# Optimization experiments

Hardware: AMD Instinct MI355X
Metric: run time of the kernel (lower is better)

Reference implementation:

```python
import jax, jax.numpy as jnp
import numpy as np

ANCHORS = np.array([[10,13],[16,30],[33,23],[30,61],[62,45],[59,119],[116,90],[156,198],[373,326]], dtype=np.float32)
MASKS = [[0,1,2],[3,4,5],[6,7,8]]
H = W = 608
NC = 80
B = 8
GRIDS = [76, 38, 19]
POS_PER_SCALE = 40


def setup_inputs() -> dict:
    key = jax.random.key(0)
    ks = jax.random.split(key, 3)
    rng = np.random.default_rng(0)
    inp = {}
    truths = []
    for i, g in enumerate(GRIDS):
        inp[f"y_out{i}"] = jax.random.normal(ks[i], (B, g, g, 3 * (5 + NC)), dtype=jnp.float32)
        t = rng.random((B, g, g, 3, 5 + NC)).astype(np.float32)
        t[..., 4] = 0.0  # objectness flag: mostly background
        flat = rng.choice(B * g * g * 3, size=POS_PER_SCALE, replace=False)
        bi, yi, xi, ai = np.unravel_index(flat, (B, g, g, 3))
        t[bi, yi, xi, ai, 4] = 1.0
        truths.append(t)
        inp[f"y_truth{i}"] = jnp.asarray(t)
    # same math as the torch code: concat over scales of truth boxes where obj==1
    gtb = np.concatenate([t[t[..., 4] == 1][:, :4] for t in truths], axis=0)
    inp["gtboxes"] = jnp.asarray(gtb)  # (120, 4)
    return inp


def _process(y, mask_idx):
    # decode raw net output -> (b, gy, gx, 3, 5+NC) normalized boxes + sigmoided obj/cls
    b, gy, gx, _ = y.shape
    out = y.reshape(b, gy, gx, 3, 5 + NC)
    a = jnp.asarray(ANCHORS[MASKS[mask_idx]])  # (3, 2)
    xx = jnp.arange(gx, dtype=y.dtype)[None, None, :, None]
    yy = jnp.arange(gy, dtype=y.dtype)[None, :, None, None]
    px = (jax.nn.sigmoid(out[..., 0]) + xx) / gx
    py = (jax.nn.sigmoid(out[..., 1]) + yy) / gy
    pw = jnp.exp(out[..., 2]) * a[:, 0] / W
    ph = jnp.exp(out[..., 3]) * a[:, 1] / H
    pobj = jax.nn.sigmoid(out[..., 4])
    pcls = jax.nn.sigmoid(out[..., 5:])
    return jnp.concatenate([px[..., None], py[..., None], pw[..., None], ph[..., None], pobj[..., None], pcls], axis=-1)


def _bce_mean(logits, targets):
    # F.binary_cross_entropy_with_logits with default reduction='mean' (a scalar)
    return jnp.mean(jnp.maximum(logits, 0.0) - logits * targets + jnp.log1p(jnp.exp(-jnp.abs(logits))))


def _scale_loss(out, truth, gtb):
    b = out.shape[0]
    # gt corners (G,)
    gx1 = gtb[:, 0] - gtb[:, 2] / 2; gy1 = gtb[:, 1] - gtb[:, 3] / 2
    gx2 = gtb[:, 0] + gtb[:, 2] / 2; gy2 = gtb[:, 1] + gtb[:, 3] / 2
    # pred corners (b, gy, gx, 3, 1)
    px1 = (out[..., 0] - out[..., 2] / 2)[..., None]
    py1 = (out[..., 1] - out[..., 3] / 2)[..., None]
    px2 = (out[..., 0] + out[..., 2] / 2)[..., None]
    py2 = (out[..., 1] + out[..., 3] / 2)[..., None]
    iw = jnp.minimum(gx2, px2) - jnp.maximum(gx1, px1)
    ih = jnp.minimum(gy2, py2) - jnp.maximum(gy1, py1)
    inter = iw * ih  # (b, gy, gx, 3, G); no clamp, faithful to source
    union = gtb[:, 2] * gtb[:, 3] + (out[..., 2] * out[..., 3])[..., None]
    iou = inter / (union - inter)
    # assign_mask: cell==global argmax of iou for any gt box
    assign = jnp.any(iou == jnp.max(iou, axis=(0, 1, 2, 3)), axis=-1).astype(out.dtype)
    obj_m = truth[..., 4]
    bls = 2.0 - truth[..., 2] * truth[..., 3]
    wgt = (assign * bls)[..., None]
    xy = jnp.sum((truth[..., :2] - out[..., :2]) ** 2 * wgt) / b
    wh = 0.5 * jnp.sum((truth[..., 2:4] - out[..., 2:4]) ** 2 * wgt) / b
    ob = _bce_mean(out[..., 4], obj_m)  # scalar, per source semantics
    objl = jnp.sum(obj_m * ob + (1.0 - assign) * (1.0 - obj_m) * ob) / b
    cb = _bce_mean(out[..., 5:], truth[..., 5:])  # scalar
    cl = jnp.sum(obj_m) * cb / b
    return xy + wh + objl + cl


def reference(y_out0, y_out1, y_out2, y_truth0, y_truth1, y_truth2, gtboxes):
    loss = jnp.float32(0.0)
    for i, (yo, yt) in enumerate([(y_out0, y_truth0), (y_out1, y_truth1), (y_out2, y_truth2)]):
        loss = loss + _scale_loss(_process(yo, i), yt, gtboxes)
    return loss
```

## Files before the change

### kernel.cpp

```cpp
#include <hip/hip_runtime.h>
#include <math.h>

#define GMAX 128

enum {
    NP0 = 138624, NP1 = 34656, NP2 = 8664,
    PB0 = (NP0 + 255) / 256,
    PB1 = (NP1 + 255) / 256,
    PB2 = (NP2 + 255) / 256,
    PBT = PB0 + PB1 + PB2,
    NE0 = NP0 * 85, NE1 = NP1 * 85, NE2 = NP2 * 85,
    NQ0 = NE0 / 4, NQ1 = NE1 / 4, NQ2 = NE2 / 4,
    SB0 = 1560, SB1 = 390, SB2 = 98,
    SBT = SB0 + SB1 + SB2
};

__constant__ float c_aw[3][3] = {{10.f,16.f,33.f},{30.f,62.f,59.f},{116.f,156.f,373.f}};
__constant__ float c_ah[3][3] = {{13.f,30.f,23.f},{61.f,45.f,119.f},{90.f,198.f,326.f}};

__device__ __forceinline__ unsigned fkey(float f) {
    unsigned u = __float_as_uint(f);
    return (u & 0x80000000u) ? ~u : (u | 0x80000000u);
}
__device__ __forceinline__ float sigm_rn(float v) {
    return __fdiv_rn(1.0f, __fadd_rn(1.0f, expf(-v)));
}
__device__ __forceinline__ float iou_rn(float px1, float py1, float px2, float py2, float pa,
                                        float gx1, float gy1, float gx2, float gy2, float ga) {
    float iw = __fsub_rn(fminf(gx2, px2), fmaxf(gx1, px1));
    float ih = __fsub_rn(fminf(gy2, py2), fmaxf(gy1, py1));
    float inter = __fmul_rn(iw, ih);
    float uni = __fadd_rn(ga, pa);
    return __fdiv_rn(inter, __fsub_rn(uni, inter));
}
__device__ __forceinline__ void decode_box(const float* __restrict__ o, int xg, int yg, float fg,
                                           float aw, float ah,
                                           float& px, float& py, float& pw, float& ph,
                                           float& x1, float& y1, float& x2, float& y2, float& pa) {
    px = __fdiv_rn(__fadd_rn(sigm_rn(o[0]), (float)xg), fg);
    py = __fdiv_rn(__fadd_rn(sigm_rn(o[1]), (float)yg), fg);
    pw = __fdiv_rn(__fmul_rn(expf(o[2]), aw), 608.0f);
    ph = __fdiv_rn(__fmul_rn(expf(o[3]), ah), 608.0f);
    float hw = __fmul_rn(pw, 0.5f), hh = __fmul_rn(ph, 0.5f);
    x1 = __fsub_rn(px, hw); x2 = __fadd_rn(px, hw);
    y1 = __fsub_rn(py, hh); y2 = __fadd_rn(py, hh);
    pa = __fmul_rn(pw, ph);
}
__device__ __forceinline__ void stage_gt(const float* __restrict__ gtb, int G, float* sg) {
    for (int t = threadIdx.x; t < G; t += blockDim.x) {
        float cx = gtb[t*4+0], cy = gtb[t*4+1], w = gtb[t*4+2], h = gtb[t*4+3];
        float hw = __fmul_rn(w, 0.5f), hh = __fmul_rn(h, 0.5f);
        sg[t*5+0] = __fsub_rn(cx, hw);
        sg[t*5+1] = __fsub_rn(cy, hh);
        sg[t*5+2] = __fadd_rn(cx, hw);
        sg[t*5+3] = __fadd_rn(cy, hh);
        sg[t*5+4] = __fmul_rn(w, h);
    }
}
__device__ __forceinline__ void bce4(float4 o, float4 t, int r0,
                                     float& bo, float& om, float& bc) {
    float ov[4] = {o.x, o.y, o.z, o.w};
    float tv[4] = {t.x, t.y, t.z, t.w};
#pragma unroll
    for (int j = 0; j < 4; j++) {
        int r = r0 + j; if (r >= 85) r -= 85;
        if (r >= 4) {
            float x = __fdividef(1.f, 1.f + __expf(-ov[j]));
            float fx = __fmaf_rn(__fmaf_rn(__fmaf_rn(-0.0088613f, x, 0.1296426f),
                                           x, -0.5006668f), x, 0.6931472f);
            float b = __fmaf_rn(-x, tv[j], x) + fx;
            if (r == 4) { bo += b; om += tv[j]; }
            else        { bc += b; }
        }
    }
}

__global__ __launch_bounds__(256) void k_zero(unsigned long long* __restrict__ gkeys) {
    for (int t = threadIdx.x; t < 3 * GMAX; t += 256) gkeys[t] = 0ull;
}

__global__ __launch_bounds__(256) void k_main(const float* __restrict__ yo0, const float* __restrict__ yt0,
                                              const float* __restrict__ yo1, const float* __restrict__ yt1,
                                              const float* __restrict__ yo2, const float* __restrict__ yt2,
                                              const float* __restrict__ gtb, int G,
                                              unsigned long long* __restrict__ gkeys,
                                              float* __restrict__ partial) {
    int bid = blockIdx.x;
    if (bid < PBT) {
        __shared__ float sg[GMAX * 5];
        __shared__ unsigned long long smax[GMAX];
        int s, lb, gd, npos;
        if (bid < PB0)            { s = 0; lb = bid;             gd = 76; npos = NP0; }
        else if (bid < PB0 + PB1) { s = 1; lb = bid - PB0;       gd = 38; npos = NP1; }
        else                      { s = 2; lb = bid - PB0 - PB1; gd = 19; npos = NP2; }
        const float* yo = (s == 0) ? yo0 : ((s == 1) ? yo1 : yo2);

        stage_gt(gtb, G, sg);
        for (int t = threadIdx.x; t < G; t += 256) smax[t] = 0ull;
        __syncthreads();

        int p = lb * 256 + threadIdx.x;
        if (p < npos) {
            int a = p % 3;
            int q = p / 3;
            int xg = q % gd;
            int yg = (q / gd) % gd;
            float px, py, pw, ph, x1, y1, x2, y2, pa;
            decode_box(yo + (size_t)p * 85, xg, yg, (float)gd, c_aw[s][a], c_ah[s][a],
                       px, py, pw, ph, x1, y1, x2, y2, pa);
            int gi = threadIdx.x % G;
            for (int i = 0; i < G; i++) {
                const float* sp = sg + gi * 5;
                float v = iou_rn(x1, y1, x2, y2, pa, sp[0], sp[1], sp[2], sp[3], sp[4]);
                atomicMax(&smax[gi], ((unsigned long long)fkey(v) << 32) | (unsigned)p);
                gi++; if (gi == G) gi = 0;
            }
        }
        __syncthreads();
        for (int t = threadIdx.x; t < G; t += 256)
            atomicMax(&gkeys[s * GMAX + t], smax[t]);
        return;
    }

    int sbid = bid - PBT;
    int s, b0, nb, nq;
    const float* yo; const float* yt;
    if (sbid < SB0)            { s = 0; b0 = sbid;             nb = SB0; yo = yo0; yt = yt0; nq = NQ0; }
    else if (sbid < SB0 + SB1) { s = 1; b0 = sbid - SB0;       nb = SB1; yo = yo1; yt = yt1; nq = NQ1; }
    else                       { s = 2; b0 = sbid - SB0 - SB1; nb = SB2; yo = yo2; yt = yt2; nq = NQ2; }
    (void)s;

    const float4* __restrict__ po = reinterpret_cast<const float4*>(yo);
    const float4* __restrict__ pt = reinterpret_cast<const float4*>(yt);
    int half = (nq + 1) >> 1;
    int stride = nb * 256;
    float bo = 0.f, om = 0.f, bc = 0.f;
    for (int qi = b0 * 256 + threadIdx.x; qi < half; qi += stride) {
        int q2 = qi + half;
        bool v2 = q2 < nq;
        int qc = v2 ? q2 : qi;
        float4 o1 = po[qi], t1 = pt[qi];
        float4 o2 = po[qc], t2 = pt[qc];
        bce4(o1, t1, (qi * 4) % 85, bo, om, bc);
        if (v2) bce4(o2, t2, (q2 * 4) % 85, bo, om, bc);
    }

    for (int off = 32; off > 0; off >>= 1) {
        bo += __shfl_down(bo, off);
        om += __shfl_down(om, off);
        bc += __shfl_down(bc, off);
    }
    __shared__ float sred[3][4];
    int wid = threadIdx.x >> 6, lane = threadIdx.x & 63;
    if (lane == 0) { sred[0][wid] = bo; sred[1][wid] = om; sred[2][wid] = bc; }
    __syncthreads();
    if (threadIdx.x == 0) {
        partial[sbid * 4 + 0] = sred[0][0] + sred[0][1] + sred[0][2] + sred[0][3];
        partial[sbid * 4 + 1] = sred[1][0] + sred[1][1] + sred[1][2] + sred[1][3];
        partial[sbid * 4 + 2] = sred[2][0] + sred[2][1] + sred[2][2] + sred[2][3];
    }
}

__global__ __launch_bounds__(256) void k_final(const float* __restrict__ yo0, const float* __restrict__ yt0,
                                               const float* __restrict__ yo1, const float* __restrict__ yt1,
                                               const float* __restrict__ yo2, const float* __restrict__ yt2,
                                               int G,
                                               const unsigned long long* __restrict__ gkeys,
                                               const float* __restrict__ partial,
                                               float* __restrict__ out) {
    __shared__ unsigned spos[3 * GMAX];
    __shared__ float sacc[9];
    __shared__ float sred[9][4];
    int tid = threadIdx.x;

    for (int t = tid; t < 3 * GMAX; t += 256) {
        unsigned long long k = gkeys[t];
        spos[t] = (k == 0ull) ? 0xffffffffu : (unsigned)(k & 0xffffffffu);
    }
    if (tid < 9) sacc[tid] = 0.f;
    __syncthreads();

    float s0b = 0.f, s0m = 0.f, s0c = 0.f;
    float s1b = 0.f, s1m = 0.f, s1c = 0.f;
    float s2b = 0.f, s2m = 0.f, s2c = 0.f;
    for (int i = tid; i < SBT; i += 256) {
        float b = partial[i * 4 + 0], m = partial[i * 4 + 1], c = partial[i * 4 + 2];
        if (i < SB0)            { s0b += b; s0m += m; s0c += c; }
        else if (i < SB0 + SB1) { s1b += b; s1m += m; s1c += c; }
        else                    { s2b += b; s2m += m; s2c += c; }
    }
    for (int off = 32; off > 0; off >>= 1) {
        s0b += __shfl_down(s0b, off); s0m += __shfl_down(s0m, off); s0c += __shfl_down(s0c, off);
        s1b += __shfl_down(s1b, off); s1m += __shfl_down(s1m, off); s1c += __shfl_down(s1c, off);
        s2b += __shfl_down(s2b, off); s2m += __shfl_down(s2m, off); s2c += __shfl_down(s2c, off);
    }
    int wid = tid >> 6, lane = tid & 63;
    if (lane == 0) {
        sred[0][wid] = s0b; sred[1][wid] = s0m; sred[2][wid] = s0c;
        sred[3][wid] = s1b; sred[4][wid] = s1m; sred[5][wid] = s1c;
        sred[6][wid] = s2b; sred[7][wid] = s2m; sred[8][wid] = s2c;
    }

    for (int t = tid; t < 3 * GMAX; t += 256) {
        unsigned pos = spos[t];
        if (pos != 0xffffffffu) {
            int s = t >> 7;
            int gi = t & (GMAX - 1);
            int base = s << 7;
            bool uniq = true;
            for (int j = 0; j < gi; j++)
                uniq = uniq && (spos[base + j] != pos);
            if (uniq) {
                const float* yo = (s == 0) ? yo0 : ((s == 1) ? yo1 : yo2);
                const float* yt = (s == 0) ? yt0 : ((s == 1) ? yt1 : yt2);
                int gd = (s == 0) ? 76 : ((s == 1) ? 38 : 19);
                int p = (int)pos;
                int a = p % 3;
                int q = p / 3;
                int xg = q % gd;
                int yg = (q / gd) % gd;
                float px, py, pw, ph, x1, y1, x2, y2, pa;
                decode_box(yo + (size_t)p * 85, xg, yg, (float)gd, c_aw[s][a], c_ah[s][a],
                           px, py, pw, ph, x1, y1, x2, y2, pa);
                const float* tp = yt + (size_t)p * 85;
                float t0 = tp[0], t1 = tp[1], t2 = tp[2], t3 = tp[3], t4 = tp[4];
                float bls = 2.0f - t2 * t3;
                float dx = t0 - px, dy = t1 - py, dw = t2 - pw, dh = t3 - ph;
                atomicAdd(&sacc[s * 3 + 0], (dx * dx + dy * dy) * bls);
                atomicAdd(&sacc[s * 3 + 1], (dw * dw + dh * dh) * bls);
                atomicAdd(&sacc[s * 3 + 2], 1.0f - t4);
            }
        }
    }
    __syncthreads();

    if (tid == 0) {
        float bos[3], oms[3], bcs[3];
        bos[0] = sred[0][0]+sred[0][1]+sred[0][2]+sred[0][3];
        oms[0] = sred[1][0]+sred[1][1]+sred[1][2]+sred[1][3];
        bcs[0] = sred[2][0]+sred[2][1]+sred[2][2]+sred[2][3];
        bos[1] = sred[3][0]+sred[3][1]+sred[3][2]+sred[3][3];
        oms[1] = sred[4][0]+sred[4][1]+sred[4][2]+sred[4][3];
        bcs[1] = sred[5][0]+sred[5][1]+sred[5][2]+sred[5][3];
        bos[2] = sred[6][0]+sred[6][1]+sred[6][2]+sred[6][3];
        oms[2] = sred[7][0]+sred[7][1]+sred[7][2]+sred[7][3];
        bcs[2] = sred[8][0]+sred[8][1]+sred[8][2]+sred[8][3];
        const float nposf[3] = {(float)NP0, (float)NP1, (float)NP2};
        float loss = 0.f;
        for (int s = 0; s < 3; s++) {
            float xy = sacc[s * 3 + 0], wh = sacc[s * 3 + 1], sc = sacc[s * 3 + 2];
            float np_ = nposf[s];
            float ob = bos[s] / np_;
            float cb = bcs[s] / (np_ * 80.f);
            loss += xy / 8.f + 0.5f * wh / 8.f + ob * (np_ - sc) / 8.f + oms[s] * cb / 8.f;
        }
        out[0] = loss;
    }
}

extern "C" void kernel_launch(void* const* d_in, const int* in_sizes, int n_in,
                              void* d_out, int out_size, void* d_ws, size_t ws_size,
                              hipStream_t stream) {
    const float *yo0, *yt0, *yo1, *yt1, *yo2, *yt2;
    if (in_sizes[0] == in_sizes[1]) {
        yo0 = (const float*)d_in[0]; yt0 = (const float*)d_in[1];
        yo1 = (const float*)d_in[2]; yt1 = (const float*)d_in[3];
        yo2 = (const float*)d_in[4]; yt2 = (const float*)d_in[5];
    } else {
        yo0 = (const float*)d_in[0]; yo1 = (const float*)d_in[1]; yo2 = (const float*)d_in[2];
        yt0 = (const float*)d_in[3]; yt1 = (const float*)d_in[4]; yt2 = (const float*)d_in[5];
    }
    const float* gtb = (const float*)d_in[6];
    int G = in_sizes[6] / 4;
    if (G > GMAX) G = GMAX;

    unsigned long long* gkeys = (unsigned long long*)d_ws;
    float* partial = (float*)((char*)d_ws + 3 * GMAX * sizeof(unsigned long long));

    k_zero <<<1, 256, 0, stream>>>(gkeys);
    k_main <<<PBT + SBT, 256, 0, stream>>>(yo0, yt0, yo1, yt1, yo2, yt2, gtb, G, gkeys, partial);
    k_final<<<1, 256, 0, stream>>>(yo0, yt0, yo1, yt1, yo2, yt2, G, gkeys, partial, (float*)d_out);
}
```

Measured before the change: 69.02 us.

## Sum BCE over all channels uniformly and subtract box/obj terms computed per anchor

The streaming BCE pass no longer computes a modulo-85 channel index per element. It now sums BCE over every element, including the four box channels and the objectness channel. The per-anchor IoU blocks compute BCE for channels 0-4 and write those sums to a second partial buffer, and the final kernel subtracts them to recover the class and objectness terms. Separately, the IoU and decode math moves from round-to-nearest intrinsics and exact division to fast approximate division and exp. This could change which box wins the argmax tie-break and slightly shift the subtracted sums.

Result: no change. 69.80 us (+1.1%).

```diff
diff --git a/kernel.cpp b/kernel.cpp
--- a/kernel.cpp
+++ b/kernel.cpp
@@ -22,56 +22,48 @@
     unsigned u = __float_as_uint(f);
     return (u & 0x80000000u) ? ~u : (u | 0x80000000u);
 }
-__device__ __forceinline__ float sigm_rn(float v) {
-    return __fdiv_rn(1.0f, __fadd_rn(1.0f, expf(-v)));
-}
-__device__ __forceinline__ float iou_rn(float px1, float py1, float px2, float py2, float pa,
-                                        float gx1, float gy1, float gx2, float gy2, float ga) {
-    float iw = __fsub_rn(fminf(gx2, px2), fmaxf(gx1, px1));
-    float ih = __fsub_rn(fminf(gy2, py2), fmaxf(gy1, py1));
-    float inter = __fmul_rn(iw, ih);
-    float uni = __fadd_rn(ga, pa);
-    return __fdiv_rn(inter, __fsub_rn(uni, inter));
-}
-__device__ __forceinline__ void decode_box(const float* __restrict__ o, int xg, int yg, float fg,
+__device__ __forceinline__ float sigm(float v) {
+    return __fdividef(1.0f, 1.0f + __expf(-v));
+}
+__device__ __forceinline__ float bce1(float v, float t) {
+    float x = sigm(v);
+    float fx = __fmaf_rn(__fmaf_rn(__fmaf_rn(-0.0088613f, x, 0.1296426f),
+                                   x, -0.5006668f), x, 0.6931472f);
+    return __fmaf_rn(-x, t, x) + fx;
+}
+__device__ __forceinline__ float bce4u(float4 o, float4 t) {
+    return bce1(o.x, t.x) + bce1(o.y, t.y) + bce1(o.z, t.z) + bce1(o.w, t.w);
+}
+__device__ __forceinline__ float iou_f(float px1, float py1, float px2, float py2, float pa,
+                                       float gx1, float gy1, float gx2, float gy2, float ga) {
+    float iw = fminf(gx2, px2) - fmaxf(gx1, px1);
+    float ih = fminf(gy2, py2) - fmaxf(gy1, py1);
+    float inter = iw * ih;
+    float uni = ga + pa;
+    return __fdividef(inter, uni - inter);
+}
+__device__ __forceinline__ void decode_box(const float* __restrict__ o, int xg, int yg, float fginv,
                                            float aw, float ah,
                                            float& px, float& py, float& pw, float& ph,
                                            float& x1, float& y1, float& x2, float& y2, float& pa) {
-    px = __fdiv_rn(__fadd_rn(sigm_rn(o[0]), (float)xg), fg);
-    py = __fdiv_rn(__fadd_rn(sigm_rn(o[1]), (float)yg), fg);
-    pw = __fdiv_rn(__fmul_rn(expf(o[2]), aw), 608.0f);
-    ph = __fdiv_rn(__fmul_rn(expf(o[3]), ah), 608.0f);
-    float hw = __fmul_rn(pw, 0.5f), hh = __fmul_rn(ph, 0.5f);
-    x1 = __fsub_rn(px, hw); x2 = __fadd_rn(px, hw);
-    y1 = __fsub_rn(py, hh); y2 = __fadd_rn(py, hh);
-    pa = __fmul_rn(pw, ph);
+    px = (sigm(o[0]) + (float)xg) * fginv;
+    py = (sigm(o[1]) + (float)yg) * fginv;
+    pw = __expf(o[2]) * aw * (1.0f / 608.0f);
+    ph = __expf(o[3]) * ah * (1.0f / 608.0f);
+    float hw = pw * 0.5f, hh = ph * 0.5f;
+    x1 = px - hw; x2 = px + hw;
+    y1 = py - hh; y2 = py + hh;
+    pa = pw * ph;
 }
 __device__ __forceinline__ void stage_gt(const float* __restrict__ gtb, int G, float* sg) {
     for (int t = threadIdx.x; t < G; t += blockDim.x) {
         float cx = gtb[t*4+0], cy = gtb[t*4+1], w = gtb[t*4+2], h = gtb[t*4+3];
-        float hw = __fmul_rn(w, 0.5f), hh = __fmul_rn(h, 0.5f);
-        sg[t*5+0] = __fsub_rn(cx, hw);
-        sg[t*5+1] = __fsub_rn(cy, hh);
-        sg[t*5+2] = __fadd_rn(cx, hw);
-        sg[t*5+3] = __fadd_rn(cy, hh);
-        sg[t*5+4] = __fmul_rn(w, h);
-    }
-}
-__device__ __forceinline__ void bce4(float4 o, float4 t, int r0,
-                                     float& bo, float& om, float& bc) {
-    float ov[4] = {o.x, o.y, o.z, o.w};
-    float tv[4] = {t.x, t.y, t.z, t.w};
-#pragma unroll
-    for (int j = 0; j < 4; j++) {
-        int r = r0 + j; if (r >= 85) r -= 85;
-        if (r >= 4) {
-            float x = __fdividef(1.f, 1.f + __expf(-ov[j]));
-            float fx = __fmaf_rn(__fmaf_rn(__fmaf_rn(-0.0088613f, x, 0.1296426f),
-                                           x, -0.5006668f), x, 0.6931472f);
-            float b = __fmaf_rn(-x, tv[j], x) + fx;
-            if (r == 4) { bo += b; om += tv[j]; }
-            else        { bc += b; }
-        }
+        float hw = w * 0.5f, hh = h * 0.5f;
+        sg[t*5+0] = cx - hw;
+        sg[t*5+1] = cy - hh;
+        sg[t*5+2] = cx + hw;
+        sg[t*5+3] = cy + hh;
+        sg[t*5+4] = w * h;
     }
 }
 
@@ -84,34 +76,47 @@
                                               const float* __restrict__ yo2, const float* __restrict__ yt2,
                                               const float* __restrict__ gtb, int G,
                                               unsigned long long* __restrict__ gkeys,
-                                              float* __restrict__ partial) {
+                                              float* __restrict__ partial,
+                                              float* __restrict__ partial2) {
     int bid = blockIdx.x;
     if (bid < PBT) {
         __shared__ float sg[GMAX * 5];
         __shared__ unsigned long long smax[GMAX];
+        __shared__ float sr2[3][4];
         int s, lb, gd, npos;
         if (bid < PB0)            { s = 0; lb = bid;             gd = 76; npos = NP0; }
         else if (bid < PB0 + PB1) { s = 1; lb = bid - PB0;       gd = 38; npos = NP1; }
         else                      { s = 2; lb = bid - PB0 - PB1; gd = 19; npos = NP2; }
         const float* yo = (s == 0) ? yo0 : ((s == 1) ? yo1 : yo2);
+        const float* yt = (s == 0) ? yt0 : ((s == 1) ? yt1 : yt2);
 
         stage_gt(gtb, G, sg);
         for (int t = threadIdx.x; t < G; t += 256) smax[t] = 0ull;
         __syncthreads();
 
+        float corrT = 0.f, b4 = 0.f, m4 = 0.f;
         int p = lb * 256 + threadIdx.x;
         if (p < npos) {
+            const float* op = yo + (size_t)p * 85;
+            const float* tp = yt + (size_t)p * 85;
+            float o0 = op[0], o1 = op[1], o2 = op[2], o3 = op[3], o4 = op[4];
+            float t0 = tp[0], t1 = tp[1], t2 = tp[2], t3 = tp[3], t4 = tp[4];
+            corrT = bce1(o0, t0) + bce1(o1, t1) + bce1(o2, t2) + bce1(o3, t3);
+            b4 = bce1(o4, t4);
+            corrT += b4;
+            m4 = t4;
+
             int a = p % 3;
             int q = p / 3;
             int xg = q % gd;
             int yg = (q / gd) % gd;
             float px, py, pw, ph, x1, y1, x2, y2, pa;
-            decode_box(yo + (size_t)p * 85, xg, yg, (float)gd, c_aw[s][a], c_ah[s][a],
+            decode_box(op, xg, yg, __fdividef(1.f, (float)gd), c_aw[s][a], c_ah[s][a],
                        px, py, pw, ph, x1, y1, x2, y2, pa);
             int gi = threadIdx.x % G;
             for (int i = 0; i < G; i++) {
                 const float* sp = sg + gi * 5;
-                float v = iou_rn(x1, y1, x2, y2, pa, sp[0], sp[1], sp[2], sp[3], sp[4]);
+                float v = iou_f(x1, y1, x2, y2, pa, sp[0], sp[1], sp[2], sp[3], sp[4]);
                 atomicMax(&smax[gi], ((unsigned long long)fkey(v) << 32) | (unsigned)p);
                 gi++; if (gi == G) gi = 0;
             }
@@ -119,46 +124,52 @@
         __syncthreads();
         for (int t = threadIdx.x; t < G; t += 256)
             atomicMax(&gkeys[s * GMAX + t], smax[t]);
+
+        for (int off = 32; off > 0; off >>= 1) {
+            corrT += __shfl_down(corrT, off);
+            b4    += __shfl_down(b4, off);
+            m4    += __shfl_down(m4, off);
+        }
+        int wid = threadIdx.x >> 6, lane = threadIdx.x & 63;
+        if (lane == 0) { sr2[0][wid] = corrT; sr2[1][wid] = b4; sr2[2][wid] = m4; }
+        __syncthreads();
+        if (threadIdx.x == 0) {
+            partial2[bid * 4 + 0] = sr2[0][0] + sr2[0][1] + sr2[0][2] + sr2[0][3];
+            partial2[bid * 4 + 1] = sr2[1][0] + sr2[1][1] + sr2[1][2] + sr2[1][3];
+            partial2[bid * 4 + 2] = sr2[2][0] + sr2[2][1] + sr2[2][2] + sr2[2][3];
+        }
         return;
     }
 
     int sbid = bid - PBT;
-    int s, b0, nb, nq;
+    int b0, nb, nq;
     const float* yo; const float* yt;
-    if (sbid < SB0)            { s = 0; b0 = sbid;             nb = SB0; yo = yo0; yt = yt0; nq = NQ0; }
-    else if (sbid < SB0 + SB1) { s = 1; b0 = sbid - SB0;       nb = SB1; yo = yo1; yt = yt1; nq = NQ1; }
-    else                       { s = 2; b0 = sbid - SB0 - SB1; nb = SB2; yo = yo2; yt = yt2; nq = NQ2; }
-    (void)s;
+    if (sbid < SB0)            { b0 = sbid;             nb = SB0; yo = yo0; yt = yt0; nq = NQ0; }
+    else if (sbid < SB0 + SB1) { b0 = sbid - SB0;       nb = SB1; yo = yo1; yt = yt1; nq = NQ1; }
+    else                       { b0 = sbid - SB0 - SB1; nb = SB2; yo = yo2; yt = yt2; nq = NQ2; }
 
     const float4* __restrict__ po = reinterpret_cast<const float4*>(yo);
     const float4* __restrict__ pt = reinterpret_cast<const float4*>(yt);
     int half = (nq + 1) >> 1;
     int stride = nb * 256;
-    float bo = 0.f, om = 0.f, bc = 0.f;
+    float acc = 0.f;
     for (int qi = b0 * 256 + threadIdx.x; qi < half; qi += stride) {
         int q2 = qi + half;
         bool v2 = q2 < nq;
         int qc = v2 ? q2 : qi;
         float4 o1 = po[qi], t1 = pt[qi];
         float4 o2 = po[qc], t2 = pt[qc];
-        bce4(o1, t1, (qi * 4) % 85, bo, om, bc);
-        if (v2) bce4(o2, t2, (q2 * 4) % 85, bo, om, bc);
-    }
-
-    for (int off = 32; off > 0; off >>= 1) {
-        bo += __shfl_down(bo, off);
-        om += __shfl_down(om, off);
-        bc += __shfl_down(bc, off);
-    }
-    __shared__ float sred[3][4];
+        acc += bce4u(o1, t1);
+        if (v2) acc += bce4u(o2, t2);
+    }
+
+    for (int off = 32; off > 0; off >>= 1) acc += __shfl_down(acc, off);
+    __shared__ float sred[4];
     int wid = threadIdx.x >> 6, lane = threadIdx.x & 63;
-    if (lane == 0) { sred[0][wid] = bo; sred[1][wid] = om; sred[2][wid] = bc; }
+    if (lane == 0) sred[wid] = acc;
     __syncthreads();
-    if (threadIdx.x == 0) {
-        partial[sbid * 4 + 0] = sred[0][0] + sred[0][1] + sred[0][2] + sred[0][3];
-        partial[sbid * 4 + 1] = sred[1][0] + sred[1][1] + sred[1][2] + sred[1][3];
-        partial[sbid * 4 + 2] = sred[2][0] + sred[2][1] + sred[2][2] + sred[2][3];
-    }
+    if (threadIdx.x == 0)
+        partial[sbid] = sred[0] + sred[1] + sred[2] + sred[3];
 }
 
 __global__ __launch_bounds__(256) void k_final(const float* __restrict__ yo0, const float* __restrict__ yt0,
@@ -167,10 +178,11 @@
                                                int G,
                                                const unsigned long long* __restrict__ gkeys,
                                                const float* __restrict__ partial,
+                                               const float* __restrict__ partial2,
                                                float* __restrict__ out) {
     __shared__ unsigned spos[3 * GMAX];
     __shared__ float sacc[9];
-    __shared__ float sred[9][4];
+    __shared__ float sred[12][4];
     int tid = threadIdx.x;
 
     for (int t = tid; t < 3 * GMAX; t += 256) {
@@ -180,25 +192,34 @@
     if (tid < 9) sacc[tid] = 0.f;
     __syncthreads();
 
-    float s0b = 0.f, s0m = 0.f, s0c = 0.f;
-    float s1b = 0.f, s1m = 0.f, s1c = 0.f;
-    float s2b = 0.f, s2m = 0.f, s2c = 0.f;
+    float S0 = 0.f, S1 = 0.f, S2 = 0.f;
+    float C0 = 0.f, C1 = 0.f, C2 = 0.f;
+    float B0 = 0.f, B1 = 0.f, B2 = 0.f;
+    float M0 = 0.f, M1 = 0.f, M2 = 0.f;
     for (int i = tid; i < SBT; i += 256) {
-        float b = partial[i * 4 + 0], m = partial[i * 4 + 1], c = partial[i * 4 + 2];
-        if (i < SB0)            { s0b += b; s0m += m; s0c += c; }
-        else if (i < SB0 + SB1) { s1b += b; s1m += m; s1c += c; }
-        else                    { s2b += b; s2m += m; s2c += c; }
+        float v = partial[i];
+        if (i < SB0)            S0 += v;
+        else if (i < SB0 + SB1) S1 += v;
+        else                    S2 += v;
+    }
+    for (int i = tid; i < PBT; i += 256) {
+        float c = partial2[i * 4 + 0], b = partial2[i * 4 + 1], m = partial2[i * 4 + 2];
+        if (i < PB0)            { C0 += c; B0 += b; M0 += m; }
+        else if (i < PB0 + PB1) { C1 += c; B1 += b; M1 += m; }
+        else                    { C2 += c; B2 += b; M2 += m; }
     }
     for (int off = 32; off > 0; off >>= 1) {
-        s0b += __shfl_down(s0b, off); s0m += __shfl_down(s0m, off); s0c += __shfl_down(s0c, off);
-        s1b += __shfl_down(s1b, off); s1m += __shfl_down(s1m, off); s1c += __shfl_down(s1c, off);
-        s2b += __shfl_down(s2b, off); s2m += __shfl_down(s2m, off); s2c += __shfl_down(s2c, off);
+        S0 += __shfl_down(S0, off); S1 += __shfl_down(S1, off); S2 += __shfl_down(S2, off);
+        C0 += __shfl_down(C0, off); C1 += __shfl_down(C1, off); C2 += __shfl_down(C2, off);
+        B0 += __shfl_down(B0, off); B1 += __shfl_down(B1, off); B2 += __shfl_down(B2, off);
+        M0 += __shfl_down(M0, off); M1 += __shfl_down(M1, off); M2 += __shfl_down(M2, off);
     }
     int wid = tid >> 6, lane = tid & 63;
     if (lane == 0) {
-        sred[0][wid] = s0b; sred[1][wid] = s0m; sred[2][wid] = s0c;
-        sred[3][wid] = s1b; sred[4][wid] = s1m; sred[5][wid] = s1c;
-        sred[6][wid] = s2b; sred[7][wid] = s2m; sred[8][wid] = s2c;
+        sred[0][wid] = S0;  sred[1][wid] = S1;  sred[2][wid] = S2;
+        sred[3][wid] = C0;  sred[4][wid] = C1;  sred[5][wid] = C2;
+        sred[6][wid] = B0;  sred[7][wid] = B1;  sred[8][wid] = B2;
+        sred[9][wid] = M0;  sred[10][wid] = M1; sred[11][wid] = M2;
     }
 
     for (int t = tid; t < 3 * GMAX; t += 256) {
@@ -220,7 +241,8 @@
                 int xg = q % gd;
                 int yg = (q / gd) % gd;
                 float px, py, pw, ph, x1, y1, x2, y2, pa;
-                decode_box(yo + (size_t)p * 85, xg, yg, (float)gd, c_aw[s][a], c_ah[s][a],
+                decode_box(yo + (size_t)p * 85, xg, yg, __fdividef(1.f, (float)gd),
+                           c_aw[s][a], c_ah[s][a],
                            px, py, pw, ph, x1, y1, x2, y2, pa);
                 const float* tp = yt + (size_t)p * 85;
                 float t0 = tp[0], t1 = tp[1], t2 = tp[2], t3 = tp[3], t4 = tp[4];
@@ -235,24 +257,21 @@
     __syncthreads();
 
     if (tid == 0) {
-        float bos[3], oms[3], bcs[3];
-        bos[0] = sred[0][0]+sred[0][1]+sred[0][2]+sred[0][3];
-        oms[0] = sred[1][0]+sred[1][1]+sred[1][2]+sred[1][3];
-        bcs[0] = sred[2][0]+sred[2][1]+sred[2][2]+sred[2][3];
-        bos[1] = sred[3][0]+sred[3][1]+sred[3][2]+sred[3][3];
-        oms[1] = sred[4][0]+sred[4][1]+sred[4][2]+sred[4][3];
-        bcs[1] = sred[5][0]+sred[5][1]+sred[5][2]+sred[5][3];
-        bos[2] = sred[6][0]+sred[6][1]+sred[6][2]+sred[6][3];
-        oms[2] = sred[7][0]+sred[7][1]+sred[7][2]+sred[7][3];
-        bcs[2] = sred[8][0]+sred[8][1]+sred[8][2]+sred[8][3];
         const float nposf[3] = {(float)NP0, (float)NP1, (float)NP2};
         float loss = 0.f;
         for (int s = 0; s < 3; s++) {
+            float S = sred[0 + s][0] + sred[0 + s][1] + sred[0 + s][2] + sred[0 + s][3];
+            float C = sred[3 + s][0] + sred[3 + s][1] + sred[3 + s][2] + sred[3 + s][3];
+            float B = sred[6 + s][0] + sred[6 + s][1] + sred[6 + s][2] + sred[6 + s][3];
+            float M = sred[9 + s][0] + sred[9 + s][1] + sred[9 + s][2] + sred[9 + s][3];
             float xy = sacc[s * 3 + 0], wh = sacc[s * 3 + 1], sc = sacc[s * 3 + 2];
             float np_ = nposf[s];
-            float ob = bos[s] / np_;
-            float cb = bcs[s] / (np_ * 80.f);
-            loss += xy / 8.f + 0.5f * wh / 8.f + ob * (np_ - sc) / 8.f + oms[s] * cb / 8.f;
+            float bo = B;
+            float bc = S - C;
+            float om = M;
+            float ob = bo / np_;
+            float cb = bc / (np_ * 80.f);
+            loss += xy / 8.f + 0.5f * wh / 8.f + ob * (np_ - sc) / 8.f + om * cb / 8.f;
         }
         out[0] = loss;
     }
@@ -275,9 +294,12 @@
     if (G > GMAX) G = GMAX;
 
     unsigned long long* gkeys = (unsigned long long*)d_ws;
-    float* partial = (float*)((char*)d_ws + 3 * GMAX * sizeof(unsigned long long));
+    float* partial  = (float*)((char*)d_ws + 3 * GMAX * sizeof(unsigned long long));
+    float* partial2 = partial + SBT;
 
     k_zero <<<1, 256, 0, stream>>>(gkeys);
-    k_main <<<PBT + SBT, 256, 0, stream>>>(yo0, yt0, yo1, yt1, yo2, yt2, gtb, G, gkeys, partial);
-    k_final<<<1, 256, 0, stream>>>(yo0, yt0, yo1, yt1, yo2, yt2, G, gkeys, partial, (float*)d_out);
-}
+    k_main <<<PBT + SBT, 256, 0, stream>>>(yo0, yt0, yo1, yt1, yo2, yt2, gtb, G,
+                                           gkeys, partial, partial2);
+    k_final<<<1, 256, 0, stream>>>(yo0, yt0, yo1, yt1, yo2, yt2, G,
+                                   gkeys, partial, partial2, (float*)d_out);
+}
```
